# Performance work log

Measured on AMD Instinct MI355X. Metric: run time of the kernel, lower is better.

## Reference

```python
import jax, jax.numpy as jnp
import numpy as np

D_MODEL = 768
N_HEADS = 12
D_K = D_MODEL // N_HEADS
B, S = 4, 2048


def setup_inputs() -> dict:
    key = jax.random.key(0)
    ks = jax.random.split(key, 9)
    sc = 1.0 / np.sqrt(D_MODEL)
    return {
        "query": jax.random.normal(ks[0], (B, S, D_MODEL), jnp.float32),
        "key": jax.random.normal(ks[1], (B, S, D_MODEL), jnp.float32),
        "value": jax.random.normal(ks[2], (B, S, D_MODEL), jnp.float32),
        "W_Q": jax.random.normal(ks[3], (D_MODEL, D_MODEL), jnp.float32) * sc,
        "b_Q": jax.random.normal(ks[4], (D_MODEL,), jnp.float32) * sc,
        "W_K": jax.random.normal(ks[5], (D_MODEL, D_MODEL), jnp.float32) * sc,
        "b_K": jax.random.normal(ks[6], (D_MODEL,), jnp.float32) * sc,
        "W_V": jax.random.normal(ks[7], (D_MODEL, D_MODEL), jnp.float32) * sc,
        "b_V": jax.random.normal(ks[8], (D_MODEL,), jnp.float32) * sc,
    }


def reference(query, key, value, W_Q, b_Q, W_K, b_K, W_V, b_V):
    b = query.shape[0]
    # QKV projections -> [B, H, S, d_k]
    def split_heads(x):
        return x.reshape(b, -1, N_HEADS, D_K).transpose(0, 2, 1, 3)
    q = split_heads(query @ W_Q + b_Q)
    k = split_heads(key @ W_K + b_K)
    v = split_heads(value @ W_V + b_V)
    # scores [B, H, Sq, Sk]
    scores = jnp.einsum("bhqd,bhkd->bhqk", q, k) / np.sqrt(D_K).astype(jnp.float32)
    attn = jax.nn.softmax(scores, axis=-1)
    ctx = jnp.einsum("bhqk,bhkd->bhqd", attn, v)
    # merge heads -> [B, S, d_model]; note: original forward does NOT apply self.linear
    return ctx.transpose(0, 2, 1, 3).reshape(b, -1, N_HEADS * D_K)
```

## Files before the change

### kernel.cpp

```cpp
#include <hip/hip_runtime.h>
#include <math.h>

#define D_MODEL 768
#define NH      12
#define DK      64
#define BATCH   4
#define SEQ     2048
#define QSCALE  0.18033688011112042f
#define MFIX    10.0f

typedef _Float16 v8h __attribute__((ext_vector_type(8)));
typedef _Float16 v4h __attribute__((ext_vector_type(4)));
typedef float    v4f __attribute__((ext_vector_type(4)));
typedef int      v4i __attribute__((ext_vector_type(4)));

#define MFMA16(a, b, c) __builtin_amdgcn_mfma_f32_16x16x32_f16(a, b, c, 0, 0, 0)

__device__ __forceinline__ void async16(const void* g, void* l) {
    __builtin_amdgcn_global_load_lds(
        (const __attribute__((address_space(1))) unsigned int*)g,
        (__attribute__((address_space(3))) unsigned int*)l, 16, 0, 0);
}

#define WH_PER_Z   589824
#define XH_PER_Z   6291456
#define BH_HALVES  131072

__global__ __launch_bounds__(256) void xcvt_kernel(
    const float* __restrict__ q_in, const float* __restrict__ k_in,
    const float* __restrict__ v_in, _Float16* __restrict__ Xh)
{
    const int kt = blockIdx.x, mt = blockIdx.y, z = blockIdx.z;
    const float* X = (z == 0) ? q_in : (z == 1) ? k_in : v_in;
    _Float16* dst = Xh + (((size_t)z * 64 + mt) * 24 + kt) * 4096;
    const int t = threadIdx.x;
    __shared__ _Float16 Ah[4096];
    #pragma unroll
    for (int i = 0; i < 4; i++) {
        int f = t + i * 256;
        int m = f >> 3, kq = (f & 7) * 4;
        float4 xv = *(const float4*)&X[((size_t)mt * 128 + m) * D_MODEL +
                                       kt * 32 + kq];
        auto p0 = __builtin_amdgcn_cvt_pkrtz(xv.x, xv.y);
        auto p1 = __builtin_amdgcn_cvt_pkrtz(xv.z, xv.w);
        v4h hv; hv[0] = p0[0]; hv[1] = p0[1]; hv[2] = p1[0]; hv[3] = p1[1];
        *(v4h*)&Ah[((m >> 4) * 64 + (m & 15) + 16 * (kq >> 3)) * 8 + (kq & 7)] = hv;
    }
    __syncthreads();
    #pragma unroll
    for (int it = 0; it < 2; it++) {
        int c = t + it * 256;
        *(v8h*)&dst[c * 8] = *(v8h*)&Ah[c * 8];
    }
}

__global__ __launch_bounds__(256) void wswz_kernel(
    const float* __restrict__ Wq, const float* __restrict__ Wk,
    const float* __restrict__ Wv, _Float16* __restrict__ Wh)
{
    const int kt = blockIdx.x, nt = blockIdx.y, z = blockIdx.z;
    const float* W = (z == 0) ? Wq : (z == 1) ? Wk : Wv;
    _Float16* dst = Wh + ((size_t)z * 144 + nt * 24 + kt) * 4096;
    const int t = threadIdx.x;

    __shared__ float Wl[32][132];
    #pragma unroll
    for (int i = 0; i < 4; i++) {
        int f = t + i * 256;
        int r = f >> 5, c4 = (f & 31) * 4;
        *(float4*)&Wl[r][c4] =
            *(const float4*)&W[(size_t)(kt * 32 + r) * D_MODEL + nt * 128 + c4];
    }
    __syncthreads();
    #pragma unroll
    for (int it = 0; it < 2; it++) {
        int c = t + it * 256;
        int nsub = c >> 6, cl = c & 63;
        int n = nsub * 16 + (cl & 15);
        int k = (cl >> 4) * 8;
        v8h hv;
        #pragma unroll
        for (int j = 0; j < 8; j++) hv[j] = (_Float16)Wl[k + j][n];
        *(v8h*)&dst[c * 8] = hv;
    }
}

__global__ __launch_bounds__(256) void proj_kernel(
    const _Float16* __restrict__ Xh, const _Float16* __restrict__ Wh,
    const float* __restrict__ bq, const float* __restrict__ bk,
    const float* __restrict__ bv,
    _Float16* __restrict__ Qs, _Float16* __restrict__ Ks,
    _Float16* __restrict__ Vs)
{
    const int nt = blockIdx.x, mt = blockIdx.y, z = blockIdx.z;
    const float* bias = (z == 0) ? bq : (z == 1) ? bk : bv;
    const _Float16* Xz = Xh + ((size_t)z * 64 + mt) * 24 * 4096;
    const _Float16* Wz = Wh + ((size_t)z * 144 + nt * 24) * 4096;

    __shared__ _Float16 smem[17408];
    _Float16* Ab = smem;
    _Float16* Bb = smem + 8192;

    const int t = threadIdx.x;
    const int lane = t & 63, w = t >> 6;
    const int wm = w & 1, wn = w >> 1;
    const int l15 = lane & 15, quad = lane >> 4;

    v4f acc[4][4];
    #pragma unroll
    for (int i = 0; i < 4; i++)
        #pragma unroll
        for (int j = 0; j < 4; j++) acc[i][j] = (v4f){0.f, 0.f, 0.f, 0.f};

    async16(Xz + (size_t)t * 8,         Ab + t * 8);
    async16(Xz + (size_t)(t + 256) * 8, Ab + (t + 256) * 8);
    async16(Wz + (size_t)t * 8,         Bb + t * 8);
    async16(Wz + (size_t)(t + 256) * 8, Bb + (t + 256) * 8);

    for (int kt = 0; kt < 24; kt++) {
        const int cur = kt & 1;
        asm volatile("s_waitcnt vmcnt(0)" ::: "memory");
        __syncthreads();
        if (kt < 23) {
            const _Float16* as = Xz + (size_t)(kt + 1) * 4096;
            const _Float16* bs = Wz + (size_t)(kt + 1) * 4096;
            _Float16* ad = Ab + (1 - cur) * 4096;
            _Float16* bd = Bb + (1 - cur) * 4096;
            async16(as + (size_t)t * 8,         ad + t * 8);
            async16(as + (size_t)(t + 256) * 8, ad + (t + 256) * 8);
            async16(bs + (size_t)t * 8,         bd + t * 8);
            async16(bs + (size_t)(t + 256) * 8, bd + (t + 256) * 8);
        }
        v8h a[4], b[4];
        #pragma unroll
        for (int i = 0; i < 4; i++)
            a[i] = *(v8h*)&Ab[cur * 4096 + ((wm * 4 + i) * 64 + lane) * 8];
        #pragma unroll
        for (int j = 0; j < 4; j++)
            b[j] = *(v8h*)&Bb[cur * 4096 + ((wn * 4 + j) * 64 + lane) * 8];
        #pragma unroll
        for (int i = 0; i < 4; i++)
            #pragma unroll
            for (int j = 0; j < 4; j++)
                acc[i][j] = MFMA16(a[i], b[j], acc[i][j]);
    }

    __syncthreads();
    _Float16* C = smem;
    if (z < 2) {
        #pragma unroll
        for (int i = 0; i < 4; i++) {
            #pragma unroll
            for (int j = 0; j < 4; j++) {
                float bval = bias[nt * 128 + wn * 64 + j * 16 + l15];
                #pragma unroll
                for (int r = 0; r < 4; r++) {
                    float val = acc[i][j][r] + bval;
                    if (z == 0) val *= QSCALE;
                    C[(wm * 64 + i * 16 + quad * 4 + r) * 136 +
                      wn * 64 + j * 16 + l15] = (_Float16)val;
                }
            }
        }
    } else {
        #pragma unroll
        for (int i = 0; i < 4; i++) {
            #pragma unroll
            for (int j = 0; j < 4; j++) {
                float bval = bias[nt * 128 + wn * 64 + j * 16 + l15];
                v4h hv;
                #pragma unroll
                for (int r = 0; r < 4; r++) hv[r] = (_Float16)(acc[i][j][r] + bval);
                *(v4h*)&C[(wn * 64 + j * 16 + l15) * 136 +
                          wm * 64 + i * 16 + quad * 4] = hv;
            }
        }
    }
    __syncthreads();

    const int bb = mt >> 4;
    if (z < 2) {
        _Float16* dstT = (z == 0) ? Qs : Ks;
        #pragma unroll
        for (int it = 0; it < 8; it++) {
            int c = t + it * 256;
            int hh = c >> 10, cl = c & 1023;
            int qsub = cl >> 7, rest = cl & 127;
            int dt = rest >> 6, cc = rest & 63;
            v8h val = *(v8h*)&C[(qsub * 16 + (cc & 15)) * 136 +
                                hh * 64 + dt * 32 + (cc >> 4) * 8];
            int h = nt * 2 + hh;
            int qt = (mt & 15) * 8 + qsub;
            *(v8h*)&dstT[(size_t)(bb * NH + h) * BH_HALVES +
                         ((qt * 2 + dt) * 64 + cc) * 8] = val;
        }
    } else {
        #pragma unroll
        for (int it = 0; it < 8; it++) {
            int c = t + it * 256;
            int hh = c >> 10, cl = c & 1023;
            int j32s = cl >> 8, rest = cl & 255;
            int dt16 = rest >> 6, cc = rest & 63;
            int g = cc >> 4, d15 = cc & 15;
            const _Float16* bp =
                &C[(hh * 64 + dt16 * 16 + d15) * 136 + j32s * 32 + g * 4];
            v4h lo = *(const v4h*)bp;
            v4h hi = *(const v4h*)(bp + 16);
            v8h val;
            val[0] = lo[0]; val[1] = lo[1]; val[2] = lo[2]; val[3] = lo[3];
            val[4] = hi[0]; val[5] = hi[1]; val[6] = hi[2]; val[7] = hi[3];
            int h = nt * 2 + hh;
            int j32g = (mt & 15) * 4 + j32s;
            *(v8h*)&Vs[(size_t)(bb * NH + h) * BH_HALVES +
                       ((j32g * 4 + dt16) * 64 + cc) * 8] = val;
        }
    }
}

__global__ __launch_bounds__(256) void attn_kernel(
    const _Float16* __restrict__ Qs, const _Float16* __restrict__ Ks,
    const _Float16* __restrict__ Vs, float* __restrict__ out)
{
    const int qb = blockIdx.x, h = blockIdx.y, b = blockIdx.z;
    const int t = threadIdx.x;
    const int lane = t & 63, w = t >> 6;
    const int l15 = lane & 15, quad = lane >> 4;
    const size_t bh = (size_t)(b * NH + h);
    const _Float16* Qb = Qs + bh * BH_HALVES;
    const _Float16* Kb = Ks + bh * BH_HALVES;
    const _Float16* Vb = Vs + bh * BH_HALVES;

    __shared__ _Float16 smem[16384];
    _Float16* Kbuf = smem;
    _Float16* Vbuf = smem + 8192;

    v8h qf[2][2];
    #pragma unroll
    for (int i = 0; i < 2; i++)
        #pragma unroll
        for (int dk = 0; dk < 2; dk++) {
            int qt = qb * 8 + w * 2 + i;
            qf[i][dk] = *(const v8h*)&Qb[((qt * 2 + dk) * 64 + lane) * 8];
        }

    v8h ones;
    #pragma unroll
    for (int j = 0; j < 8; j++) ones[j] = (_Float16)1.0f;

    v4f o[2][4];
    v4f osum[2];
    #pragma unroll
    for (int i = 0; i < 2; i++) {
        osum[i] = (v4f){0.f, 0.f, 0.f, 0.f};
        #pragma unroll
        for (int dt = 0; dt < 4; dt++) o[i][dt] = (v4f){0.f, 0.f, 0.f, 0.f};
    }

    auto chunk_compute = [&](const _Float16* Kl, const _Float16* Vl) {
        v4f sc[2][4];
        #pragma unroll
        for (int i = 0; i < 2; i++)
            #pragma unroll
            for (int nt = 0; nt < 4; nt++)
                sc[i][nt] = (v4f){-MFIX, -MFIX, -MFIX, -MFIX};
        __builtin_amdgcn_s_setprio(1);
        #pragma unroll
        for (int nt = 0; nt < 4; nt++) {
            #pragma unroll
            for (int dk = 0; dk < 2; dk++) {
                v8h kf = *(v8h*)&Kl[((nt * 2 + dk) * 64 + lane) * 8];
                sc[0][nt] = MFMA16(kf, qf[0][dk], sc[0][nt]);
                sc[1][nt] = MFMA16(kf, qf[1][dk], sc[1][nt]);
            }
        }
        __builtin_amdgcn_s_setprio(0);

        v4i paw[2][2];
        #pragma unroll
        for (int i = 0; i < 2; i++) {
            #pragma unroll
            for (int nt = 0; nt < 4; nt++) {
                float p0 = __builtin_amdgcn_exp2f(sc[i][nt][0]);
                float p1 = __builtin_amdgcn_exp2f(sc[i][nt][1]);
                float p2 = __builtin_amdgcn_exp2f(sc[i][nt][2]);
                float p3 = __builtin_amdgcn_exp2f(sc[i][nt][3]);
                auto h0 = __builtin_amdgcn_cvt_pkrtz(p0, p1);
                auto h1 = __builtin_amdgcn_cvt_pkrtz(p2, p3);
                paw[i][nt >> 1][(nt & 1) * 2 + 0] = __builtin_bit_cast(int, h0);
                paw[i][nt >> 1][(nt & 1) * 2 + 1] = __builtin_bit_cast(int, h1);
            }
        }

        __builtin_amdgcn_s_setprio(1);
        #pragma unroll
        for (int mf = 0; mf < 2; mf++) {
            v8h pa0 = __builtin_bit_cast(v8h, paw[0][mf]);
            v8h pa1 = __builtin_bit_cast(v8h, paw[1][mf]);
            #pragma unroll
            for (int dt = 0; dt < 4; dt++) {
                v8h vf = *(v8h*)&Vl[((mf * 4 + dt) * 64 + lane) * 8];
                o[0][dt] = MFMA16(pa0, vf, o[0][dt]);
                o[1][dt] = MFMA16(pa1, vf, o[1][dt]);
            }
            osum[0] = MFMA16(pa0, ones, osum[0]);
            osum[1] = MFMA16(pa1, ones, osum[1]);
        }
        __builtin_amdgcn_s_setprio(0);
    };

    async16(Kb + (size_t)t * 8,         Kbuf + t * 8);
    async16(Kb + (size_t)(t + 256) * 8, Kbuf + (t + 256) * 8);
    async16(Vb + (size_t)t * 8,         Vbuf + t * 8);
    async16(Vb + (size_t)(t + 256) * 8, Vbuf + (t + 256) * 8);

    for (int c = 0; c < 32; c += 2) {
        asm volatile("s_waitcnt vmcnt(0)" ::: "memory");
        __syncthreads();
        {
            const _Float16* ks = Kb + (size_t)(c + 1) * 4096;
            const _Float16* vs = Vb + (size_t)(c + 1) * 4096;
            async16(ks + (size_t)t * 8,         Kbuf + 4096 + t * 8);
            async16(ks + (size_t)(t + 256) * 8, Kbuf + 4096 + (t + 256) * 8);
            async16(vs + (size_t)t * 8,         Vbuf + 4096 + t * 8);
            async16(vs + (size_t)(t + 256) * 8, Vbuf + 4096 + (t + 256) * 8);
        }
        chunk_compute(Kbuf, Vbuf);

        asm volatile("s_waitcnt vmcnt(0)" ::: "memory");
        __syncthreads();
        if (c < 30) {
            const _Float16* ks = Kb + (size_t)(c + 2) * 4096;
            const _Float16* vs = Vb + (size_t)(c + 2) * 4096;
            async16(ks + (size_t)t * 8,         Kbuf + t * 8);
            async16(ks + (size_t)(t + 256) * 8, Kbuf + (t + 256) * 8);
            async16(vs + (size_t)t * 8,         Vbuf + t * 8);
            async16(vs + (size_t)(t + 256) * 8, Vbuf + (t + 256) * 8);
        }
        chunk_compute(Kbuf + 4096, Vbuf + 4096);
    }

    #pragma unroll
    for (int i = 0; i < 2; i++) {
        #pragma unroll
        for (int r = 0; r < 4; r++) {
            float inv = 1.0f / osum[i][r];
            int s = qb * 128 + w * 32 + i * 16 + quad * 4 + r;
            #pragma unroll
            for (int dt = 0; dt < 4; dt++)
                out[((size_t)b * SEQ + s) * D_MODEL + h * DK + dt * 16 + l15] =
                    o[i][dt][r] * inv;
        }
    }
}

extern "C" void kernel_launch(void* const* d_in, const int* in_sizes, int n_in,
                              void* d_out, int out_size, void* d_ws, size_t ws_size,
                              hipStream_t stream)
{
    const float* q_in = (const float*)d_in[0];
    const float* k_in = (const float*)d_in[1];
    const float* v_in = (const float*)d_in[2];
    const float* Wq   = (const float*)d_in[3];
    const float* bq   = (const float*)d_in[4];
    const float* Wk   = (const float*)d_in[5];
    const float* bk   = (const float*)d_in[6];
    const float* Wv   = (const float*)d_in[7];
    const float* bv   = (const float*)d_in[8];
    float* out = (float*)d_out;

    _Float16* Wh = (_Float16*)d_ws;
    _Float16* Xh = Wh + 3 * (size_t)WH_PER_Z;
    _Float16* Qs = Xh + 3 * (size_t)XH_PER_Z;
    _Float16* Ks = Qs + (size_t)BATCH * NH * BH_HALVES;
    _Float16* Vs = Ks + (size_t)BATCH * NH * BH_HALVES;

    wswz_kernel<<<dim3(24, 6, 3), 256, 0, stream>>>(Wq, Wk, Wv, Wh);
    xcvt_kernel<<<dim3(24, 64, 3), 256, 0, stream>>>(q_in, k_in, v_in, Xh);
    proj_kernel<<<dim3(6, 64, 3), 256, 0, stream>>>(Xh, Wh, bq, bk, bv,
                                                    Qs, Ks, Vs);
    attn_kernel<<<dim3(16, NH, BATCH), 256, 0, stream>>>(Qs, Ks, Vs, out);
}
```

Baseline: 232.4 us.

## Merge prep kernels, triple-buffer proj and attention loads, remap blocks across XCDs

Folds the weight-swizzle and activation-convert kernels into one launch, so one kernel launch and its tail go away. The projection and attention main loops move from double to triple buffering with partial vmcnt waits and a single barrier per step, letting two chunks of loads stay in flight. Block indices are remapped so that neighbouring logical tiles land on the same XCD, which should improve L2 reuse. In exchange, LDS use per block grows to 48 KB, which may lower occupancy.

```diff
diff --git a/kernel.cpp b/kernel.cpp
--- a/kernel.cpp
+++ b/kernel.cpp
@@ -26,62 +26,68 @@
 #define XH_PER_Z   6291456
 #define BH_HALVES  131072
 
-__global__ __launch_bounds__(256) void xcvt_kernel(
+__global__ __launch_bounds__(256) void prep_kernel(
     const float* __restrict__ q_in, const float* __restrict__ k_in,
-    const float* __restrict__ v_in, _Float16* __restrict__ Xh)
+    const float* __restrict__ v_in,
+    const float* __restrict__ Wq, const float* __restrict__ Wk,
+    const float* __restrict__ Wv,
+    _Float16* __restrict__ Xh, _Float16* __restrict__ Wh)
 {
-    const int kt = blockIdx.x, mt = blockIdx.y, z = blockIdx.z;
-    const float* X = (z == 0) ? q_in : (z == 1) ? k_in : v_in;
-    _Float16* dst = Xh + (((size_t)z * 64 + mt) * 24 + kt) * 4096;
+    const int kt = blockIdx.x, my = blockIdx.y, z = blockIdx.z;
     const int t = threadIdx.x;
-    __shared__ _Float16 Ah[4096];
-    #pragma unroll
-    for (int i = 0; i < 4; i++) {
-        int f = t + i * 256;
-        int m = f >> 3, kq = (f & 7) * 4;
-        float4 xv = *(const float4*)&X[((size_t)mt * 128 + m) * D_MODEL +
-                                       kt * 32 + kq];
-        auto p0 = __builtin_amdgcn_cvt_pkrtz(xv.x, xv.y);
-        auto p1 = __builtin_amdgcn_cvt_pkrtz(xv.z, xv.w);
-        v4h hv; hv[0] = p0[0]; hv[1] = p0[1]; hv[2] = p1[0]; hv[3] = p1[1];
-        *(v4h*)&Ah[((m >> 4) * 64 + (m & 15) + 16 * (kq >> 3)) * 8 + (kq & 7)] = hv;
-    }
-    __syncthreads();
-    #pragma unroll
-    for (int it = 0; it < 2; it++) {
-        int c = t + it * 256;
-        *(v8h*)&dst[c * 8] = *(v8h*)&Ah[c * 8];
-    }
-}
-
-__global__ __launch_bounds__(256) void wswz_kernel(
-    const float* __restrict__ Wq, const float* __restrict__ Wk,
-    const float* __restrict__ Wv, _Float16* __restrict__ Wh)
-{
-    const int kt = blockIdx.x, nt = blockIdx.y, z = blockIdx.z;
-    const float* W = (z == 0) ? Wq : (z == 1) ? Wk : Wv;
-    _Float16* dst = Wh + ((size_t)z * 144 + nt * 24 + kt) * 4096;
-    const int t = threadIdx.x;
-
-    __shared__ float Wl[32][132];
-    #pragma unroll
-    for (int i = 0; i < 4; i++) {
-        int f = t + i * 256;
-        int r = f >> 5, c4 = (f & 31) * 4;
-        *(float4*)&Wl[r][c4] =
-            *(const float4*)&W[(size_t)(kt * 32 + r) * D_MODEL + nt * 128 + c4];
-    }
-    __syncthreads();
-    #pragma unroll
-    for (int it = 0; it < 2; it++) {
-        int c = t + it * 256;
-        int nsub = c >> 6, cl = c & 63;
-        int n = nsub * 16 + (cl & 15);
-        int k = (cl >> 4) * 8;
-        v8h hv;
-        #pragma unroll
-        for (int j = 0; j < 8; j++) hv[j] = (_Float16)Wl[k + j][n];
-        *(v8h*)&dst[c * 8] = hv;
+    __shared__ __align__(16) char smraw[32 * 132 * 4];
+
+    if (my < 64) {
+        const int mt = my;
+        _Float16* Ah = (_Float16*)smraw;
+        const float* X = (z == 0) ? q_in : (z == 1) ? k_in : v_in;
+        _Float16* dst = Xh + (((size_t)z * 64 + mt) * 24 + kt) * 4096;
+        #pragma unroll
+        for (int i = 0; i < 4; i++) {
+            int f = t + i * 256;
+            int m = f >> 3, kq = (f & 7) * 4;
+            float4 xv = *(const float4*)&X[((size_t)mt * 128 + m) * D_MODEL +
+                                           kt * 32 + kq];
+            auto p0 = __builtin_amdgcn_cvt_pkrtz(xv.x, xv.y);
+            auto p1 = __builtin_amdgcn_cvt_pkrtz(xv.z, xv.w);
+            v4h hv; hv[0] = p0[0]; hv[1] = p0[1]; hv[2] = p1[0]; hv[3] = p1[1];
+            *(v4h*)&Ah[((m >> 4) * 64 + (m & 15) + 16 * (kq >> 3)) * 8 + (kq & 7)] = hv;
+        }
+        __syncthreads();
+        #pragma unroll
+        for (int it = 0; it < 2; it++) {
+            int c = t + it * 256;
+            *(v8h*)&dst[c * 8] = *(v8h*)&Ah[c * 8];
+        }
+    } else {
+        float (*Wl)[132] = (float(*)[132])smraw;
+        const float* W = (z == 0) ? Wq : (z == 1) ? Wk : Wv;
+        const int mtx = my - 64;
+        for (int nn = 0; nn < 3; nn++) {
+            const int nt = mtx * 3 + nn;
+            _Float16* dst = Wh + ((size_t)z * 144 + nt * 24 + kt) * 4096;
+            #pragma unroll
+            for (int i = 0; i < 4; i++) {
+                int f = t + i * 256;
+                int r = f >> 5, c4 = (f & 31) * 4;
+                *(float4*)&Wl[r][c4] =
+                    *(const float4*)&W[(size_t)(kt * 32 + r) * D_MODEL +
+                                       nt * 128 + c4];
+            }
+            __syncthreads();
+            #pragma unroll
+            for (int it = 0; it < 2; it++) {
+                int c = t + it * 256;
+                int nsub = c >> 6, cl = c & 63;
+                int n = nsub * 16 + (cl & 15);
+                int k = (cl >> 4) * 8;
+                v8h hv;
+                #pragma unroll
+                for (int j = 0; j < 8; j++) hv[j] = (_Float16)Wl[k + j][n];
+                *(v8h*)&dst[c * 8] = hv;
+            }
+            __syncthreads();
+        }
     }
 }
 
@@ -92,14 +98,22 @@
     _Float16* __restrict__ Qs, _Float16* __restrict__ Ks,
     _Float16* __restrict__ Vs)
 {
-    const int nt = blockIdx.x, mt = blockIdx.y, z = blockIdx.z;
+    const int d  = blockIdx.x + 6 * (blockIdx.y + 64 * blockIdx.z);
+    const int cx = d & 7, jj = d >> 3;
+    const int g  = cx + 8 * (jj / 6);
+    const int l  = g * 6 + (jj % 6);
+    const int nt = l % 6;
+    const int mz = l / 6;
+    const int mt = mz & 63;
+    const int z  = mz >> 6;
+
     const float* bias = (z == 0) ? bq : (z == 1) ? bk : bv;
     const _Float16* Xz = Xh + ((size_t)z * 64 + mt) * 24 * 4096;
     const _Float16* Wz = Wh + ((size_t)z * 144 + nt * 24) * 4096;
 
-    __shared__ _Float16 smem[17408];
+    __shared__ _Float16 smem[24576];
     _Float16* Ab = smem;
-    _Float16* Bb = smem + 8192;
+    _Float16* Bb = smem + 12288;
 
     const int t = threadIdx.x;
     const int lane = t & 63, w = t >> 6;
@@ -112,38 +126,47 @@
         #pragma unroll
         for (int j = 0; j < 4; j++) acc[i][j] = (v4f){0.f, 0.f, 0.f, 0.f};
 
-    async16(Xz + (size_t)t * 8,         Ab + t * 8);
-    async16(Xz + (size_t)(t + 256) * 8, Ab + (t + 256) * 8);
-    async16(Wz + (size_t)t * 8,         Bb + t * 8);
-    async16(Wz + (size_t)(t + 256) * 8, Bb + (t + 256) * 8);
-
+#define STAGE_PROJ(ch, bufi) do {                                        \
+        const _Float16* as_ = Xz + (size_t)(ch) * 4096;                  \
+        const _Float16* bs_ = Wz + (size_t)(ch) * 4096;                  \
+        _Float16* ad_ = Ab + (bufi) * 4096;                              \
+        _Float16* bd_ = Bb + (bufi) * 4096;                              \
+        async16(as_ + (size_t)t * 8,         ad_ + t * 8);               \
+        async16(as_ + (size_t)(t + 256) * 8, ad_ + (t + 256) * 8);       \
+        async16(bs_ + (size_t)t * 8,         bd_ + t * 8);               \
+        async16(bs_ + (size_t)(t + 256) * 8, bd_ + (t + 256) * 8);       \
+    } while (0)
+
+    STAGE_PROJ(0, 0);
+    STAGE_PROJ(1, 1);
+
+    int buf = 0;
     for (int kt = 0; kt < 24; kt++) {
-        const int cur = kt & 1;
-        asm volatile("s_waitcnt vmcnt(0)" ::: "memory");
-        __syncthreads();
-        if (kt < 23) {
-            const _Float16* as = Xz + (size_t)(kt + 1) * 4096;
-            const _Float16* bs = Wz + (size_t)(kt + 1) * 4096;
-            _Float16* ad = Ab + (1 - cur) * 4096;
-            _Float16* bd = Bb + (1 - cur) * 4096;
-            async16(as + (size_t)t * 8,         ad + t * 8);
-            async16(as + (size_t)(t + 256) * 8, ad + (t + 256) * 8);
-            async16(bs + (size_t)t * 8,         bd + t * 8);
-            async16(bs + (size_t)(t + 256) * 8, bd + (t + 256) * 8);
-        }
+        if (kt < 23) asm volatile("s_waitcnt vmcnt(4)" ::: "memory");
+        else         asm volatile("s_waitcnt vmcnt(0)" ::: "memory");
+        __builtin_amdgcn_s_barrier();
+        asm volatile("" ::: "memory");
+        if (kt < 22) {
+            int nbuf = buf + 2; if (nbuf >= 3) nbuf -= 3;
+            STAGE_PROJ(kt + 2, nbuf);
+        }
+        const _Float16* Al = Ab + buf * 4096;
+        const _Float16* Bl = Bb + buf * 4096;
         v8h a[4], b[4];
         #pragma unroll
         for (int i = 0; i < 4; i++)
-            a[i] = *(v8h*)&Ab[cur * 4096 + ((wm * 4 + i) * 64 + lane) * 8];
+            a[i] = *(v8h*)&Al[((wm * 4 + i) * 64 + lane) * 8];
         #pragma unroll
         for (int j = 0; j < 4; j++)
-            b[j] = *(v8h*)&Bb[cur * 4096 + ((wn * 4 + j) * 64 + lane) * 8];
+            b[j] = *(v8h*)&Bl[((wn * 4 + j) * 64 + lane) * 8];
         #pragma unroll
         for (int i = 0; i < 4; i++)
             #pragma unroll
             for (int j = 0; j < 4; j++)
                 acc[i][j] = MFMA16(a[i], b[j], acc[i][j]);
-    }
+        buf = (buf == 2) ? 0 : buf + 1;
+    }
+#undef STAGE_PROJ
 
     __syncthreads();
     _Float16* C = smem;
@@ -201,9 +224,9 @@
             int hh = c >> 10, cl = c & 1023;
             int j32s = cl >> 8, rest = cl & 255;
             int dt16 = rest >> 6, cc = rest & 63;
-            int g = cc >> 4, d15 = cc & 15;
+            int gg = cc >> 4, d15 = cc & 15;
             const _Float16* bp =
-                &C[(hh * 64 + dt16 * 16 + d15) * 136 + j32s * 32 + g * 4];
+                &C[(hh * 64 + dt16 * 16 + d15) * 136 + j32s * 32 + gg * 4];
             v4h lo = *(const v4h*)bp;
             v4h hi = *(const v4h*)(bp + 16);
             v8h val;
@@ -221,7 +244,15 @@
     const _Float16* __restrict__ Qs, const _Float16* __restrict__ Ks,
     const _Float16* __restrict__ Vs, float* __restrict__ out)
 {
-    const int qb = blockIdx.x, h = blockIdx.y, b = blockIdx.z;
+    const int d  = blockIdx.x + 16 * (blockIdx.y + 12 * blockIdx.z);
+    const int cx = d & 7, jj = d >> 3;
+    const int g  = cx + 8 * (jj >> 4);
+    const int l  = g * 16 + (jj & 15);
+    const int qb = l & 15;
+    const int hb = l >> 4;
+    const int h  = hb % NH;
+    const int b  = hb / NH;
+
     const int t = threadIdx.x;
     const int lane = t & 63, w = t >> 6;
     const int l15 = lane & 15, quad = lane >> 4;
@@ -230,9 +261,9 @@
     const _Float16* Kb = Ks + bh * BH_HALVES;
     const _Float16* Vb = Vs + bh * BH_HALVES;
 
-    __shared__ _Float16 smem[16384];
+    __shared__ _Float16 smem[24576];
     _Float16* Kbuf = smem;
-    _Float16* Vbuf = smem + 8192;
+    _Float16* Vbuf = smem + 12288;
 
     v8h qf[2][2];
     #pragma unroll
@@ -242,6 +273,7 @@
             int qt = qb * 8 + w * 2 + i;
             qf[i][dk] = *(const v8h*)&Qb[((qt * 2 + dk) * 64 + lane) * 8];
         }
+    asm volatile("" ::: "memory");
 
     v8h ones;
     #pragma unroll
@@ -308,36 +340,34 @@
         __builtin_amdgcn_s_setprio(0);
     };
 
-    async16(Kb + (size_t)t * 8,         Kbuf + t * 8);
-    async16(Kb + (size_t)(t + 256) * 8, Kbuf + (t + 256) * 8);
-    async16(Vb + (size_t)t * 8,         Vbuf + t * 8);
-    async16(Vb + (size_t)(t + 256) * 8, Vbuf + (t + 256) * 8);
-
-    for (int c = 0; c < 32; c += 2) {
-        asm volatile("s_waitcnt vmcnt(0)" ::: "memory");
-        __syncthreads();
-        {
-            const _Float16* ks = Kb + (size_t)(c + 1) * 4096;
-            const _Float16* vs = Vb + (size_t)(c + 1) * 4096;
-            async16(ks + (size_t)t * 8,         Kbuf + 4096 + t * 8);
-            async16(ks + (size_t)(t + 256) * 8, Kbuf + 4096 + (t + 256) * 8);
-            async16(vs + (size_t)t * 8,         Vbuf + 4096 + t * 8);
-            async16(vs + (size_t)(t + 256) * 8, Vbuf + 4096 + (t + 256) * 8);
-        }
-        chunk_compute(Kbuf, Vbuf);
-
-        asm volatile("s_waitcnt vmcnt(0)" ::: "memory");
-        __syncthreads();
+#define STAGE_ATTN(ch, bufi) do {                                        \
+        const _Float16* ks_ = Kb + (size_t)(ch) * 4096;                  \
+        const _Float16* vs_ = Vb + (size_t)(ch) * 4096;                  \
+        _Float16* kd_ = Kbuf + (bufi) * 4096;                            \
+        _Float16* vd_ = Vbuf + (bufi) * 4096;                            \
+        async16(ks_ + (size_t)t * 8,         kd_ + t * 8);               \
+        async16(ks_ + (size_t)(t + 256) * 8, kd_ + (t + 256) * 8);       \
+        async16(vs_ + (size_t)t * 8,         vd_ + t * 8);               \
+        async16(vs_ + (size_t)(t + 256) * 8, vd_ + (t + 256) * 8);       \
+    } while (0)
+
+    STAGE_ATTN(0, 0);
+    STAGE_ATTN(1, 1);
+
+    int buf = 0;
+    for (int c = 0; c < 32; c++) {
+        if (c < 31) asm volatile("s_waitcnt vmcnt(4)" ::: "memory");
+        else        asm volatile("s_waitcnt vmcnt(0)" ::: "memory");
+        __builtin_amdgcn_s_barrier();
+        asm volatile("" ::: "memory");
         if (c < 30) {
-            const _Float16* ks = Kb + (size_t)(c + 2) * 4096;
-            const _Float16* vs = Vb + (size_t)(c + 2) * 4096;
-            async16(ks + (size_t)t * 8,         Kbuf + t * 8);
-            async16(ks + (size_t)(t + 256) * 8, Kbuf + (t + 256) * 8);
-            async16(vs + (size_t)t * 8,         Vbuf + t * 8);
-            async16(vs + (size_t)(t + 256) * 8, Vbuf + (t + 256) * 8);
-        }
-        chunk_compute(Kbuf + 4096, Vbuf + 4096);
-    }
+            int nbuf = buf + 2; if (nbuf >= 3) nbuf -= 3;
+            STAGE_ATTN(c + 2, nbuf);
+        }
+        chunk_compute(Kbuf + buf * 4096, Vbuf + buf * 4096);
+        buf = (buf == 2) ? 0 : buf + 1;
+    }
+#undef STAGE_ATTN
 
     #pragma unroll
     for (int i = 0; i < 2; i++) {
@@ -374,8 +404,8 @@
     _Float16* Ks = Qs + (size_t)BATCH * NH * BH_HALVES;
     _Float16* Vs = Ks + (size_t)BATCH * NH * BH_HALVES;
 
-    wswz_kernel<<<dim3(24, 6, 3), 256, 0, stream>>>(Wq, Wk, Wv, Wh);
-    xcvt_kernel<<<dim3(24, 64, 3), 256, 0, stream>>>(q_in, k_in, v_in, Xh);
+    prep_kernel<<<dim3(24, 66, 3), 256, 0, stream>>>(q_in, k_in, v_in,
+                                                     Wq, Wk, Wv, Xh, Wh);
     proj_kernel<<<dim3(6, 64, 3), 256, 0, stream>>>(Xh, Wh, bq, bk, bv,
                                                     Qs, Ks, Vs);
     attn_kernel<<<dim3(16, NH, BATCH), 256, 0, stream>>>(Qs, Ks, Vs, out);
```

New measurement: 235.3 us. Within noise of the previous version (+1.2%).
